# Kernel optimization log

Hardware: AMD Instinct MI355X
Metric: run time of the kernel (lower is better)

The kernel has to match this reference:

```python
import jax, jax.numpy as jnp
import numpy as np

B_GRAPHS, N_PER, T = 64, 5, 256
F_NODE, F_GLOB = 64, 16
H_MSG, H_UPD, H_GRP, H_ACT = 128, 128, 64, 4


def _lstm(x, Wih, Whh, bih, bhh):
    """PyTorch-semantics single-layer LSTM, batch_first=False.
    x: [L, B, Din] -> out [L, B, H]. Scan runs over dim 0 (faithful to the
    original code, which feeds [edges/nodes, T, F] into nn.LSTM)."""
    H = Whh.shape[1]
    xz = jnp.einsum('lbd,gd->lbg', x, Wih) + (bih + bhh)  # precomputed input proj [L,B,4H]
    h0 = jnp.zeros((x.shape[1], H), x.dtype)

    def step(carry, zt):
        h, c = carry
        z = zt + h @ Whh.T
        i, f, g, o = jnp.split(z, 4, axis=-1)  # torch gate order: i,f,g,o
        c = jax.nn.sigmoid(f) * c + jax.nn.sigmoid(i) * jnp.tanh(g)
        h = jax.nn.sigmoid(o) * jnp.tanh(c)
        return (h, c), h

    _, ys = jax.lax.scan(step, (h0, h0), xz)
    return ys


def _forward(nodes, global_attr,
             Wih_m, Whh_m, bih_m, bhh_m,
             Wih_u, Whh_u, bih_u, bhh_u,
             Wih_g, Whh_g, bih_g, bhh_g,
             Wih_a, Whh_a, bih_a, bhh_a,
             edge_indices, num_nodes, num_edges, batch_indices, chosen_who):
    N, Tdim = nodes.shape[0], nodes.shape[1]
    E = edge_indices.shape[1]
    B = num_nodes.shape[0]
    # Faithful to source: both src and target use edge_indices[0]
    src = edge_indices[0]
    tgt = edge_indices[0]
    ga = global_attr.reshape(-1, Tdim, global_attr.shape[1])  # [B, T, G]

    # --- message phase: gather -> LSTM -> relu -> scatter_min ---
    glob_e = jnp.repeat(ga, num_edges, axis=0, total_repeat_length=E)  # [E,T,G]
    msg_in = jnp.concatenate([nodes[src], nodes[tgt], glob_e], axis=2)  # [E,T,2F+G]
    message = jax.nn.relu(_lstm(msg_in, Wih_m, Whh_m, bih_m, bhh_m))    # [E,T,Hm]
    aggr = jax.ops.segment_min(message, tgt, num_segments=N)            # [N,T,Hm]

    # --- node update ---
    glob_n = jnp.repeat(ga, num_nodes, axis=0, total_repeat_length=N)   # [N,T,G]
    upd_in = jnp.concatenate([nodes, aggr, glob_n], axis=2)
    upd = jax.nn.relu(_lstm(upd_in, Wih_u, Whh_u, bih_u, bhh_u))        # [N,T,Hu]

    # --- global / group embedding ---
    agg_nodes = jax.ops.segment_min(upd, batch_indices, num_segments=B) # [B,T,Hu]
    group = jax.nn.relu(_lstm(jnp.concatenate([agg_nodes, ga], axis=2),
                              Wih_g, Whh_g, bih_g, bhh_g))              # [B,T,Hg]

    # --- action head ---
    agg_all = jax.ops.segment_min(upd, batch_indices, num_segments=B)
    counts = jax.ops.segment_sum(jnp.ones_like(batch_indices), batch_indices, num_segments=B)
    offsets = jnp.concatenate([jnp.zeros((1,), counts.dtype), jnp.cumsum(counts)[:-1]])
    adj = jnp.where(chosen_who == 3, chosen_who - 1, chosen_who)
    # faithful: element 0 is NOT adjusted/offset in the original loop
    atbw = jnp.where(jnp.arange(B) == 0, chosen_who, adj + offsets)
    chosen = upd[atbw]                                                  # [B,T,Hu]
    chosen = jnp.where((chosen_who == 3)[:, None, None], agg_all, chosen)
    act_in = jnp.concatenate([chosen, group], axis=2)                   # [B,T,Hu+Hg]
    res = _lstm(act_in, Wih_a, Whh_a, bih_a, bhh_a)[:, -1, :]           # [B, A]
    return jax.nn.softmax(res, axis=1)


def _lstm_params(k, din, h):
    k1, k2, k3, k4 = jax.random.split(k, 4)
    s = 1.0 / np.sqrt(h)
    return (jax.random.uniform(k1, (4 * h, din), jnp.float32, -s, s),
            jax.random.uniform(k2, (4 * h, h), jnp.float32, -s, s),
            jax.random.uniform(k3, (4 * h,), jnp.float32, -s, s),
            jax.random.uniform(k4, (4 * h,), jnp.float32, -s, s))


def setup_inputs() -> dict:
    key = jax.random.key(0)
    ks = jax.random.split(key, 8)
    N = B_GRAPHS * N_PER
    # complete directed graph inside each small group
    src, dst = [], []
    for g in range(B_GRAPHS):
        for i in range(N_PER):
            for j in range(N_PER):
                if i != j:
                    src.append(g * N_PER + i)
                    dst.append(g * N_PER + j)
    edge_indices = jnp.array([src, dst], dtype=jnp.int32)
    inp = {
        'nodes': jax.random.normal(ks[0], (N, T, F_NODE), jnp.float32),
        'global_attr': jax.random.normal(ks[1], (B_GRAPHS * T, F_GLOB), jnp.float32),
        'edge_indices': edge_indices,
        'num_nodes': jnp.full((B_GRAPHS,), N_PER, jnp.int32),
        'num_edges': jnp.full((B_GRAPHS,), N_PER * (N_PER - 1), jnp.int32),
        'batch_indices': jnp.repeat(jnp.arange(B_GRAPHS, dtype=jnp.int32), N_PER),
        'chosen_who': jax.random.randint(ks[2], (B_GRAPHS,), 0, 4, jnp.int32),
    }
    names = [('m', 2 * F_NODE + F_GLOB, H_MSG), ('u', H_MSG + F_NODE + F_GLOB, H_UPD),
             ('g', H_UPD + F_GLOB, H_GRP), ('a', H_UPD + H_GRP, H_ACT)]
    for idx, (suf, din, h) in enumerate(names):
        Wih, Whh, bih, bhh = _lstm_params(ks[3 + idx], din, h)
        inp['Wih_' + suf] = Wih
        inp['Whh_' + suf] = Whh
        inp['bih_' + suf] = bih
        inp['bhh_' + suf] = bhh
    return inp


def reference(nodes, global_attr, edge_indices, num_nodes, num_edges, batch_indices, chosen_who,
              Wih_m, Whh_m, bih_m, bhh_m, Wih_u, Whh_u, bih_u, bhh_u,
              Wih_g, Whh_g, bih_g, bhh_g, Wih_a, Whh_a, bih_a, bhh_a):
    return _forward(nodes, global_attr,
                    Wih_m, Whh_m, bih_m, bhh_m,
                    Wih_u, Whh_u, bih_u, bhh_u,
                    Wih_g, Whh_g, bih_g, bhh_g,
                    Wih_a, Whh_a, bih_a, bhh_a,
                    edge_indices, num_nodes, num_edges, batch_indices, chosen_who)
```

## Files before the change

kernel.cpp:

```cpp
#include <hip/hip_runtime.h>

typedef unsigned int u32;
typedef unsigned short u16;
typedef __fp16 h2 __attribute__((ext_vector_type(2)));

#define BG 64
#define NNODE 320
#define NEDGE 1280
#define TT 256
#define FN 64
#define FG 16
#define HM 128
#define HU 128
#define HG 64
#define HA 4
#define ZM 512
#define ZU 512
#define ZG 256
#define ZA 16
#define DM 144
#define DU 208
#define DG 144
#define DA 192

#define CV 64
#define O_NODES 0
#define O_GA    20480
#define O_WM    21504
#define O_WHM   95232
#define O_BM    160768
#define O_WU    161280
#define O_WHU   267776
#define O_BU    333312
#define O_WG    333824
#define O_WHG   370688
#define O_BG2   387072
#define O_WA    387328
#define O_WHA   390400
#define O_BA    390464
#define CONV_TOTAL 390480
#define O_XZN   390528
#define O_XZU   (O_XZN + NNODE * ZM)
#define O_XZG   (O_XZU + NNODE * ZU)
#define O_XZA   (O_XZG + BG * ZG)
#define O_AGGR  (O_XZA + BG * ZA)
#define O_UPD   (O_AGGR + NNODE * HM)
#define WS_FLOATS (CV + O_UPD + NNODE * HU)

__device__ __forceinline__ float bf2f(u16 v) {
  return __uint_as_float(((u32)v) << 16);
}
__device__ __forceinline__ float rcp_(float x) { return __builtin_amdgcn_rcpf(x); }
__device__ __forceinline__ float sigf(float x) { return rcp_(1.0f + __expf(-x)); }
__device__ __forceinline__ float tanh_(float x) {
  float e = __expf(-2.0f * fabsf(x));
  float t = (1.0f - e) * rcp_(1.0f + e);
  return copysignf(t, x);
}
__device__ __forceinline__ float cvt(const void* p, int i, int flag) {
  return flag ? bf2f(((const u16*)p)[i]) : ((const float*)p)[i];
}

__device__ __forceinline__ h2 pk2(float a, float b) {
  return __builtin_amdgcn_cvt_pkrtz(a, b);
}
__device__ __forceinline__ u32 pk2u(float a, float b) {
  h2 r = __builtin_amdgcn_cvt_pkrtz(a, b);
  u32 out;
  __builtin_memcpy(&out, &r, 4);
  return out;
}

__device__ __forceinline__ float fdot2_(h2 a, h2 b, float c) {
#if __has_builtin(__builtin_amdgcn_fdot2)
  return __builtin_amdgcn_fdot2(a, b, c, false);
#else
  u32 ua, ub;
  __builtin_memcpy(&ua, &a, 4);
  __builtin_memcpy(&ub, &b, 4);
  asm("v_dot2_f32_f16 %0, %1, %2, %0" : "+v"(c) : "v"(ua), "v"(ub));
  return c;
#endif
}

template <int CTRL>
__device__ __forceinline__ float dppmov(float s) {
  return __int_as_float(
      __builtin_amdgcn_update_dpp(0, __float_as_int(s), CTRL, 0xF, 0xF, true));
}

#define BAR() asm volatile("s_waitcnt lgkmcnt(0)\n\ts_barrier" ::: "memory")

__global__ void k_detect(const u32* __restrict__ raw, int* __restrict__ flagp) {
  const int t = threadIdx.x;
  int zlo = 0, hits = 0;
  for (int k = t; k < 256; k += 64) {
    u32 w = raw[k];
    if ((w & 0xFFFFu) == 0u) zlo++;
    u32 m = (w >> 8) & 0x7Fu;
    if (m >= 40u && m <= 70u) hits++;
  }
#pragma unroll
  for (int off = 32; off; off >>= 1) {
    zlo += __shfl_down(zlo, off, 64);
    hits += __shfl_down(hits, off, 64);
  }
  if (t == 0) *flagp = (zlo < 128 && hits >= 128) ? 1 : 0;
}

__global__ __launch_bounds__(256) void k_convert(
    const void* nodes, const void* gattr,
    const void* Wm, const void* Whm, const void* bm1, const void* bm2,
    const void* Wu, const void* Whu, const void* bu1, const void* bu2,
    const void* Wg, const void* Whg, const void* bg1, const void* bg2,
    const void* Wa, const void* Wha, const void* ba1, const void* ba2,
    const int* __restrict__ flagp, float* __restrict__ dst) {
  const int flag = *flagp;
  const int i = blockIdx.x * 256 + threadIdx.x;
  if (i >= CONV_TOTAL) return;
  float v;
  if (i < O_GA) {
    int n = i >> 6, f = i & 63;
    v = cvt(nodes, (n * TT + (TT - 1)) * FN + f, flag);
  } else if (i < O_WM) {
    int l = i - O_GA; int b = l >> 4, g = l & 15;
    v = cvt(gattr, (b * TT + (TT - 1)) * FG + g, flag);
  } else if (i < O_BM) {
    v = (i < O_WHM) ? cvt(Wm, i - O_WM, flag) : cvt(Whm, i - O_WHM, flag);
  } else if (i < O_WU) {
    int l = i - O_BM; v = cvt(bm1, l, flag) + cvt(bm2, l, flag);
  } else if (i < O_BU) {
    v = (i < O_WHU) ? cvt(Wu, i - O_WU, flag) : cvt(Whu, i - O_WHU, flag);
  } else if (i < O_WG) {
    int l = i - O_BU; v = cvt(bu1, l, flag) + cvt(bu2, l, flag);
  } else if (i < O_BG2) {
    v = (i < O_WHG) ? cvt(Wg, i - O_WG, flag) : cvt(Whg, i - O_WHG, flag);
  } else if (i < O_WA) {
    int l = i - O_BG2; v = cvt(bg1, l, flag) + cvt(bg2, l, flag);
  } else if (i < O_WHA) {
    v = cvt(Wa, i - O_WA, flag);
  } else if (i < O_BA) {
    v = cvt(Wha, i - O_WHA, flag);
  } else {
    int l = i - O_BA; v = cvt(ba1, l, flag) + cvt(ba2, l, flag);
  }
  dst[i] = v;
}

__global__ __launch_bounds__(256) void k_pre(
    const float* __restrict__ cva,
    const int* __restrict__ num_nodes,
    float* __restrict__ XZN, float* __restrict__ XZu, float* __restrict__ XZg,
    u32* __restrict__ aggr) {
  const int blk = blockIdx.x, tid = threadIdx.x;
  __shared__ float xv[FN];
  __shared__ float gav[FG];
  __shared__ int sgr;
  const float* nodes255 = cva + O_NODES;
  const float* ga255 = cva + O_GA;

  if (blk < NNODE) {
    const int n = blk;
    if (tid < HM) aggr[(size_t)n * HM + tid] = 0x7f800000u;
    if (tid == 0) {
      int g = 0, acc = 0;
      while (g < BG) { int c = num_nodes[g]; if (n < acc + c) break; acc += c; ++g; }
      if (g >= BG) g = BG - 1;
      sgr = g;
    }
    if (tid < FN) xv[tid] = nodes255[n * FN + tid];
    __syncthreads();
    if (tid < FG) gav[tid] = ga255[sgr * FG + tid];
    __syncthreads();
    for (int j = tid; j < ZM; j += 256) {
      const float* wr = cva + O_WM + j * DM;
      float acc = cva[O_BM + j];
#pragma unroll
      for (int d = 0; d < FN; ++d) acc += (wr[d] + wr[FN + d]) * xv[d];
#pragma unroll
      for (int d = 0; d < FG; ++d) acc += wr[2 * FN + d] * gav[d];
      XZN[(size_t)n * ZM + j] = acc;
    }
  } else if (blk < 2 * NNODE) {
    const int n = blk - NNODE;
    if (tid == 0) {
      int g = 0, acc = 0;
      while (g < BG) { int c = num_nodes[g]; if (n < acc + c) break; acc += c; ++g; }
      if (g >= BG) g = BG - 1;
      sgr = g;
    }
    if (tid < FN) xv[tid] = nodes255[n * FN + tid];
    __syncthreads();
    if (tid < FG) gav[tid] = ga255[sgr * FG + tid];
    __syncthreads();
    for (int j = tid; j < ZU; j += 256) {
      const float* wr = cva + O_WU + j * DU;
      float acc = cva[O_BU + j];
#pragma unroll
      for (int d = 0; d < FN; ++d) acc += wr[d] * xv[d];
#pragma unroll
      for (int d = 0; d < FG; ++d) acc += wr[FN + HM + d] * gav[d];
      XZu[(size_t)n * ZU + j] = acc;
    }
  } else {
    const int b = blk - 2 * NNODE;
    if (tid < FG) gav[tid] = ga255[b * FG + tid];
    __syncthreads();
    if (tid < ZG) {
      const float* wr = cva + O_WG + tid * DG;
      float acc = cva[O_BG2 + tid];
#pragma unroll
      for (int d = 0; d < FG; ++d) acc += wr[HU + d] * gav[d];
      XZg[(size_t)b * ZG + tid] = acc;
    }
  }
}

template <int STEPS, bool GATHER, bool ATOMIN>
__global__ __launch_bounds__(512, 2) void k_chain(
    const float* __restrict__ Whh, const float* __restrict__ XZ,
    const int* __restrict__ idx, float* __restrict__ hout) {
  const int t = threadIdx.x;
  const int p = t & 3;
  const int elem = t >> 2;
  const bool islead = (p == 0);
  __shared__ u32 hbuf[2][80];

  h2 w16[64];
  {
    const float4* wr = (const float4*)(Whh + (size_t)(p * 128 + elem) * 128);
#pragma unroll
    for (int q = 0; q < 32; ++q) {
      float4 v = wr[q];
      w16[2 * q] = pk2(v.x, v.y);
      w16[2 * q + 1] = pk2(v.z, v.w);
    }
  }
  const float LOG2E = 1.4426950408889634f;
  const float kmul = (p == 2) ? (-2.0f * LOG2E) : (-LOG2E);
  const float smul = (p == 2) ? 2.0f : 1.0f;
  const float badd = (p == 2) ? -1.0f : 0.0f;
  const float KT2 = -2.0f * LOG2E;

  if (t < 160) ((u32*)hbuf)[t] = 0u;
  float c = 0.0f;
  float hrelu_prev = 0.0f;
  int crow = GATHER ? idx[0] : 0;
  float xz = XZ[(size_t)crow * 512 + p * 128 + elem];
  int nrow = GATHER ? idx[1] : 1;
  BAR();
  int cur = 0;
  for (int e = 0; e < STEPS; ++e) {
    const uint4* hb = (const uint4*)&hbuf[cur][0];
    float a0 = 0.0f, a1 = 0.0f, a2 = 0.0f, a3 = 0.0f;
#pragma unroll
    for (int q = 0; q < 16; ++q) {
      uint4 tv = hb[q];
      h2 h0, h1, h2_, h3;
      __builtin_memcpy(&h0, &tv.x, 4);
      __builtin_memcpy(&h1, &tv.y, 4);
      __builtin_memcpy(&h2_, &tv.z, 4);
      __builtin_memcpy(&h3, &tv.w, 4);
      a0 = fdot2_(w16[4 * q + 0], h0, a0);
      a1 = fdot2_(w16[4 * q + 1], h1, a1);
      a2 = fdot2_(w16[4 * q + 2], h2_, a2);
      a3 = fdot2_(w16[4 * q + 3], h3, a3);
    }
    float z = ((a0 + a1) + (a2 + a3)) + xz;
    float xzn = XZ[(size_t)nrow * 512 + p * 128 + elem];
    int crow_next = nrow;
    nrow = GATHER ? idx[e + 2] : (e + 2);
    float ex = __builtin_amdgcn_exp2f(z * kmul);
    float gq = __builtin_fmaf(smul, rcp_(1.0f + ex), badd);
    float gf = dppmov<0xB1>(gq);
    float gt = dppmov<0x4E>(gq);
    float go = dppmov<0x1B>(gq);
    c = __builtin_fmaf(gf, c, gq * gt);
    float ec = __builtin_amdgcn_exp2f(c * KT2);
    float th = __builtin_fmaf(2.0f, rcp_(1.0f + ec), -1.0f);
    float h = go * th;
    if (islead) {
      ((u16*)&hbuf[cur ^ 1][0])[elem] = (u16)pk2u(h, h);
      float hr = fmaxf(h, 0.0f);
      if (ATOMIN) {
        atomicMin((u32*)&hout[(size_t)crow * HM + elem], __float_as_uint(hr));
      } else {
        if (e > 0) hout[(size_t)(e - 1) * 128 + elem] = hrelu_prev;
        hrelu_prev = hr;
      }
    }
    crow = crow_next;
    xz = xzn;
    BAR();
    cur ^= 1;
  }
  if (islead && !ATOMIN) hout[(size_t)(STEPS - 1) * 128 + elem] = hrelu_prev;
}

__global__ __launch_bounds__(256) void k_aggproj(
    const float* __restrict__ cva, const float* __restrict__ aggr,
    float* __restrict__ XZu) {
  const int n = blockIdx.x, tid = threadIdx.x;
  __shared__ float av[HM];
  if (tid < HM) av[tid] = aggr[(size_t)n * HM + tid];
  __syncthreads();
  for (int j = tid; j < ZU; j += 256) {
    const float* wr = cva + O_WU + j * DU + FN;
    float acc = 0.0f;
#pragma unroll
    for (int k = 0; k < HM; ++k) acc += wr[k] * av[k];
    XZu[(size_t)n * ZU + j] += acc;
  }
}

__global__ __launch_bounds__(256) void k_gproj(
    const float* __restrict__ cva, const float* __restrict__ upd,
    const int* __restrict__ bidx, const int* __restrict__ who,
    float* __restrict__ XZg, float* __restrict__ XZa) {
  const int blk = blockIdx.x, tid = threadIdx.x;
  __shared__ float buf[HU];
  __shared__ int satbw;
  if (blk < BG) {
    const int b = blk;
    if (tid < HU) {
      float m = __uint_as_float(0x7f800000u);
      for (int n = 0; n < NNODE; ++n) {
        if (bidx[n] == b) m = fminf(m, upd[(size_t)n * HU + tid]);
      }
      buf[tid] = m;
    }
    __syncthreads();
    if (tid < ZG) {
      const float* wr = cva + O_WG + tid * DG;
      float acc = 0.0f;
#pragma unroll
      for (int k = 0; k < HU; ++k) acc += wr[k] * buf[k];
      XZg[(size_t)b * ZG + tid] += acc;
    }
  } else {
    const int b = blk - BG;
    const int whoB = who[b];
    if (tid == 0) {
      int off = 0;
      for (int i = 0; i < NNODE; ++i) off += (bidx[i] < b) ? 1 : 0;
      const int adj = (whoB == 3) ? 2 : whoB;
      satbw = (b == 0) ? who[0] : (adj + off);
    }
    if (whoB == 3) {
      if (tid < HU) {
        float m = __uint_as_float(0x7f800000u);
        for (int n = 0; n < NNODE; ++n) {
          if (bidx[n] == b) m = fminf(m, upd[(size_t)n * HU + tid]);
        }
        buf[tid] = m;
      }
      __syncthreads();
    } else {
      __syncthreads();
      if (tid < HU) buf[tid] = upd[(size_t)satbw * HU + tid];
      __syncthreads();
    }
    if (tid < ZA) {
      const float* wr = cva + O_WA + tid * DA;
      float acc = cva[O_BA + tid];
#pragma unroll
      for (int k = 0; k < HU; ++k) acc += wr[k] * buf[k];
      XZa[(size_t)b * ZA + tid] = acc;
    }
  }
}

__global__ __launch_bounds__(256, 2) void k_final(
    const float* __restrict__ cva, const float* __restrict__ XZg,
    const float* __restrict__ XZa, float* __restrict__ out) {
  const int j = threadIdx.x;
  __shared__ __align__(16) float hg[HG];
  __shared__ float zsg[ZG];
  __shared__ float grp[BG * HG];
  __shared__ float za[ZA];
  __shared__ float haL[HA];
  __shared__ float res[BG * HA];

  float wg[HG];
  {
    const float* wr = cva + O_WHG + j * HG;
#pragma unroll
    for (int k = 0; k < HG; ++k) wg[k] = wr[k];
  }
  float wa2[HG];
  float wha[HA];
  if (j < ZA) {
    const float* wr2 = cva + O_WA + j * DA + HU;
#pragma unroll
    for (int k = 0; k < HG; ++k) wa2[k] = wr2[k];
#pragma unroll
    for (int k = 0; k < HA; ++k) wha[k] = cva[O_WHA + j * HA + k];
  }
  if (j < HG) hg[j] = 0.0f;
  if (j < HA) haL[j] = 0.0f;
  float cg = 0.0f, ca = 0.0f;
  __syncthreads();

  for (int b = 0; b <= BG; ++b) {
    if (b < BG) {
      float acc = XZg[(size_t)b * ZG + j];
#pragma unroll
      for (int k = 0; k < HG; ++k) acc += wg[k] * hg[k];
      zsg[j] = acc;
    }
    if (b > 0 && j < ZA) {
      float acc = XZa[(size_t)(b - 1) * ZA + j];
#pragma unroll
      for (int k = 0; k < HG; ++k) acc += wa2[k] * grp[(b - 1) * HG + k];
#pragma unroll
      for (int k = 0; k < HA; ++k) acc += wha[k] * haL[k];
      za[j] = acc;
    }
    __syncthreads();
    if (b < BG && j < HG) {
      float zi = zsg[j], zf = zsg[HG + j], zg = zsg[2 * HG + j], zo = zsg[3 * HG + j];
      cg = sigf(zf) * cg + sigf(zi) * tanh_(zg);
      float h = sigf(zo) * tanh_(cg);
      hg[j] = h;
      grp[b * HG + j] = fmaxf(h, 0.0f);
    }
    if (b > 0 && j < HA) {
      float zi = za[j], zf = za[HA + j], zg = za[2 * HA + j], zo = za[3 * HA + j];
      ca = sigf(zf) * ca + sigf(zi) * tanh_(zg);
      float h = sigf(zo) * tanh_(ca);
      haL[j] = h;
      res[(b - 1) * HA + j] = h;
    }
    __syncthreads();
  }

  if (j < BG) {
    float x0 = res[j * 4 + 0], x1 = res[j * 4 + 1];
    float x2 = res[j * 4 + 2], x3 = res[j * 4 + 3];
    float m = fmaxf(fmaxf(x0, x1), fmaxf(x2, x3));
    float e0 = __expf(x0 - m), e1 = __expf(x1 - m);
    float e2 = __expf(x2 - m), e3 = __expf(x3 - m);
    float s = e0 + e1 + e2 + e3;
    out[j * 4 + 0] = e0 / s;
    out[j * 4 + 1] = e1 / s;
    out[j * 4 + 2] = e2 / s;
    out[j * 4 + 3] = e3 / s;
  }
}

__global__ void k_zero(float* out) { out[threadIdx.x] = 0.0f; }

extern "C" void kernel_launch(void* const* d_in, const int* in_sizes, int n_in,
                              void* d_out, int out_size, void* d_ws, size_t ws_size,
                              hipStream_t stream) {
  const void* nodes = d_in[0];
  const void* gattr = d_in[1];
  const int* eidx  = (const int*)d_in[2];
  const int* nn    = (const int*)d_in[3];
  const int* ne    = (const int*)d_in[4];
  const int* bidx  = (const int*)d_in[5];
  const int* who   = (const int*)d_in[6];
  (void)ne;

  if (ws_size < (size_t)WS_FLOATS * 4) {
    k_zero<<<1, 256, 0, stream>>>((float*)d_out);
    return;
  }

  float* ws = (float*)d_ws;
  int* flagp = (int*)d_ws;
  float* cva = ws + CV;
  float* XZN = cva + O_XZN;
  float* XZu = cva + O_XZU;
  float* XZg = cva + O_XZG;
  float* XZa = cva + O_XZA;
  float* aggr = cva + O_AGGR;
  float* upd = cva + O_UPD;

  k_detect<<<1, 64, 0, stream>>>((const u32*)nodes, flagp);
  k_convert<<<(CONV_TOTAL + 255) / 256, 256, 0, stream>>>(
      nodes, gattr,
      d_in[7], d_in[8], d_in[9], d_in[10],
      d_in[11], d_in[12], d_in[13], d_in[14],
      d_in[15], d_in[16], d_in[17], d_in[18],
      d_in[19], d_in[20], d_in[21], d_in[22],
      flagp, cva);
  k_pre<<<2 * NNODE + BG, 256, 0, stream>>>(cva, nn, XZN, XZu, XZg, (u32*)aggr);
  k_chain<NEDGE, true, true><<<1, 512, 0, stream>>>(cva + O_WHM, XZN, eidx, aggr);
  k_aggproj<<<NNODE, 256, 0, stream>>>(cva, aggr, XZu);
  k_chain<NNODE, false, false><<<1, 512, 0, stream>>>(cva + O_WHU, XZu, nullptr, upd);
  k_gproj<<<2 * BG, 256, 0, stream>>>(cva, upd, bidx, who, XZg, XZa);
  k_final<<<1, 256, 0, stream>>>(cva, XZg, XZa, (float*)d_out);
}
```

Before: 1.124 ms.

## Compute LSTM recurrent matvec with MFMA and interleave gate layout

Replaces the per-thread fdot2 recurrent matvec in the sequential LSTM chain kernel with MFMA 16x16x32 f16 instructions. The weights are held as A fragments and the hidden vector is broadcast as the B operand. Gate pre-activations go through shared memory to 128 cell threads, and the XZ projections are stored gate-interleaved so each cell thread loads its four gates as one float4. This adds a second barrier per step and wastes most MFMA columns (only one useful column). Latency per step may improve or worsen.

```diff
diff --git a/kernel.cpp b/kernel.cpp
--- a/kernel.cpp
+++ b/kernel.cpp
@@ -2,7 +2,8 @@
 
 typedef unsigned int u32;
 typedef unsigned short u16;
-typedef __fp16 h2 __attribute__((ext_vector_type(2)));
+typedef __fp16 h8 __attribute__((ext_vector_type(8)));
+typedef float f32x4 __attribute__((ext_vector_type(4)));
 
 #define BG 64
 #define NNODE 320
@@ -60,33 +61,11 @@
 __device__ __forceinline__ float cvt(const void* p, int i, int flag) {
   return flag ? bf2f(((const u16*)p)[i]) : ((const float*)p)[i];
 }
-
-__device__ __forceinline__ h2 pk2(float a, float b) {
-  return __builtin_amdgcn_cvt_pkrtz(a, b);
-}
-__device__ __forceinline__ u32 pk2u(float a, float b) {
-  h2 r = __builtin_amdgcn_cvt_pkrtz(a, b);
+__device__ __forceinline__ u16 f2h(float a) {
+  auto r = __builtin_amdgcn_cvt_pkrtz(a, a);
   u32 out;
   __builtin_memcpy(&out, &r, 4);
-  return out;
-}
-
-__device__ __forceinline__ float fdot2_(h2 a, h2 b, float c) {
-#if __has_builtin(__builtin_amdgcn_fdot2)
-  return __builtin_amdgcn_fdot2(a, b, c, false);
-#else
-  u32 ua, ub;
-  __builtin_memcpy(&ua, &a, 4);
-  __builtin_memcpy(&ub, &b, 4);
-  asm("v_dot2_f32_f16 %0, %1, %2, %0" : "+v"(c) : "v"(ua), "v"(ub));
-  return c;
-#endif
-}
-
-template <int CTRL>
-__device__ __forceinline__ float dppmov(float s) {
-  return __int_as_float(
-      __builtin_amdgcn_update_dpp(0, __float_as_int(s), CTRL, 0xF, 0xF, true));
+  return (u16)out;
 }
 
 #define BAR() asm volatile("s_waitcnt lgkmcnt(0)\n\ts_barrier" ::: "memory")
@@ -179,7 +158,7 @@
       for (int d = 0; d < FN; ++d) acc += (wr[d] + wr[FN + d]) * xv[d];
 #pragma unroll
       for (int d = 0; d < FG; ++d) acc += wr[2 * FN + d] * gav[d];
-      XZN[(size_t)n * ZM + j] = acc;
+      XZN[(size_t)n * ZM + (j & 127) * 4 + (j >> 7)] = acc;
     }
   } else if (blk < 2 * NNODE) {
     const int n = blk - NNODE;
@@ -200,7 +179,7 @@
       for (int d = 0; d < FN; ++d) acc += wr[d] * xv[d];
 #pragma unroll
       for (int d = 0; d < FG; ++d) acc += wr[FN + HM + d] * gav[d];
-      XZu[(size_t)n * ZU + j] = acc;
+      XZu[(size_t)n * ZU + (j & 127) * 4 + (j >> 7)] = acc;
     }
   } else {
     const int b = blk - 2 * NNODE;
@@ -221,80 +200,95 @@
     const float* __restrict__ Whh, const float* __restrict__ XZ,
     const int* __restrict__ idx, float* __restrict__ hout) {
   const int t = threadIdx.x;
-  const int p = t & 3;
-  const int elem = t >> 2;
-  const bool islead = (p == 0);
-  __shared__ u32 hbuf[2][80];
-
-  h2 w16[64];
+  const int lane = t & 63;
+  const int wv = t >> 6;
+  const bool iscell = (t < 128);
+  __shared__ __align__(16) u16 hlds[136];
+  __shared__ __align__(16) float zlds[512];
+
+  h8 wfrag[16];
   {
-    const float4* wr = (const float4*)(Whh + (size_t)(p * 128 + elem) * 128);
-#pragma unroll
-    for (int q = 0; q < 32; ++q) {
-      float4 v = wr[q];
-      w16[2 * q] = pk2(v.x, v.y);
-      w16[2 * q + 1] = pk2(v.z, v.w);
-    }
-  }
-  const float LOG2E = 1.4426950408889634f;
-  const float kmul = (p == 2) ? (-2.0f * LOG2E) : (-LOG2E);
-  const float smul = (p == 2) ? 2.0f : 1.0f;
-  const float badd = (p == 2) ? -1.0f : 0.0f;
-  const float KT2 = -2.0f * LOG2E;
-
-  if (t < 160) ((u32*)hbuf)[t] = 0u;
-  float c = 0.0f;
-  float hrelu_prev = 0.0f;
-  int crow = GATHER ? idx[0] : 0;
-  float xz = XZ[(size_t)crow * 512 + p * 128 + elem];
-  int nrow = GATHER ? idx[1] : 1;
+    const int vr = lane & 15;
+    const int kb = (lane >> 4) * 8;
+#pragma unroll
+    for (int mm = 0; mm < 4; ++mm) {
+      const int m = wv * 4 + mm;
+      const int vrow = 16 * m + vr;
+      const int elem = vrow >> 2;
+      const int p = vrow & 3;
+      const float* row = Whh + (size_t)(p * 128 + elem) * 128;
+#pragma unroll
+      for (int c = 0; c < 4; ++c) {
+        float4 lo = *(const float4*)(row + 32 * c + kb);
+        float4 hi = *(const float4*)(row + 32 * c + kb + 4);
+        h8 f;
+        f[0] = (__fp16)lo.x; f[1] = (__fp16)lo.y;
+        f[2] = (__fp16)lo.z; f[3] = (__fp16)lo.w;
+        f[4] = (__fp16)hi.x; f[5] = (__fp16)hi.y;
+        f[6] = (__fp16)hi.z; f[7] = (__fp16)hi.w;
+        wfrag[mm * 4 + c] = f;
+      }
+    }
+  }
+
+  float cst = 0.0f;
+  int crow = 0, nrow = 1;
+  f32x4 xz = {0.0f, 0.0f, 0.0f, 0.0f};
+  if (iscell) {
+    crow = GATHER ? idx[0] : 0;
+    nrow = GATHER ? idx[1] : 1;
+    xz = *(const f32x4*)(XZ + (size_t)crow * 512 + t * 4);
+  }
+  if (t < 136) hlds[t] = 0;
   BAR();
-  int cur = 0;
+
   for (int e = 0; e < STEPS; ++e) {
-    const uint4* hb = (const uint4*)&hbuf[cur][0];
-    float a0 = 0.0f, a1 = 0.0f, a2 = 0.0f, a3 = 0.0f;
-#pragma unroll
-    for (int q = 0; q < 16; ++q) {
-      uint4 tv = hb[q];
-      h2 h0, h1, h2_, h3;
-      __builtin_memcpy(&h0, &tv.x, 4);
-      __builtin_memcpy(&h1, &tv.y, 4);
-      __builtin_memcpy(&h2_, &tv.z, 4);
-      __builtin_memcpy(&h3, &tv.w, 4);
-      a0 = fdot2_(w16[4 * q + 0], h0, a0);
-      a1 = fdot2_(w16[4 * q + 1], h1, a1);
-      a2 = fdot2_(w16[4 * q + 2], h2_, a2);
-      a3 = fdot2_(w16[4 * q + 3], h3, a3);
-    }
-    float z = ((a0 + a1) + (a2 + a3)) + xz;
-    float xzn = XZ[(size_t)nrow * 512 + p * 128 + elem];
-    int crow_next = nrow;
-    nrow = GATHER ? idx[e + 2] : (e + 2);
-    float ex = __builtin_amdgcn_exp2f(z * kmul);
-    float gq = __builtin_fmaf(smul, rcp_(1.0f + ex), badd);
-    float gf = dppmov<0xB1>(gq);
-    float gt = dppmov<0x4E>(gq);
-    float go = dppmov<0x1B>(gq);
-    c = __builtin_fmaf(gf, c, gq * gt);
-    float ec = __builtin_amdgcn_exp2f(c * KT2);
-    float th = __builtin_fmaf(2.0f, rcp_(1.0f + ec), -1.0f);
-    float h = go * th;
-    if (islead) {
-      ((u16*)&hbuf[cur ^ 1][0])[elem] = (u16)pk2u(h, h);
+    h8 bf[4];
+#pragma unroll
+    for (int c = 0; c < 4; ++c) {
+      uint4 v = *(const uint4*)((const char*)hlds + 64 * c + ((lane >> 4) & 3) * 16);
+      __builtin_memcpy(&bf[c], &v, 16);
+    }
+    f32x4 d0 = {0.0f, 0.0f, 0.0f, 0.0f};
+    f32x4 d1 = d0, d2 = d0, d3 = d0;
+#pragma unroll
+    for (int c = 0; c < 4; ++c) {
+      d0 = __builtin_amdgcn_mfma_f32_16x16x32_f16(wfrag[0 * 4 + c], bf[c], d0, 0, 0, 0);
+      d1 = __builtin_amdgcn_mfma_f32_16x16x32_f16(wfrag[1 * 4 + c], bf[c], d1, 0, 0, 0);
+      d2 = __builtin_amdgcn_mfma_f32_16x16x32_f16(wfrag[2 * 4 + c], bf[c], d2, 0, 0, 0);
+      d3 = __builtin_amdgcn_mfma_f32_16x16x32_f16(wfrag[3 * 4 + c], bf[c], d3, 0, 0, 0);
+    }
+    if ((lane & 15) == 0) {
+      const int rb = (lane >> 4) * 4;
+      *(f32x4*)&zlds[16 * (wv * 4 + 0) + rb] = d0;
+      *(f32x4*)&zlds[16 * (wv * 4 + 1) + rb] = d1;
+      *(f32x4*)&zlds[16 * (wv * 4 + 2) + rb] = d2;
+      *(f32x4*)&zlds[16 * (wv * 4 + 3) + rb] = d3;
+    }
+    BAR();
+    if (iscell) {
+      f32x4 z = *(const f32x4*)&zlds[t * 4];
+      float zi = z[0] + xz[0], zf = z[1] + xz[1];
+      float zg = z[2] + xz[2], zo = z[3] + xz[3];
+      int crow_next = nrow;
+      f32x4 xzn = *(const f32x4*)(XZ + (size_t)nrow * 512 + t * 4);
+      nrow = GATHER ? idx[e + 2] : (e + 2);
+      float si = sigf(zi), sf = sigf(zf), so = sigf(zo);
+      float tg = tanh_(zg);
+      cst = sf * cst + si * tg;
+      float h = so * tanh_(cst);
+      hlds[t] = f2h(h);
       float hr = fmaxf(h, 0.0f);
       if (ATOMIN) {
-        atomicMin((u32*)&hout[(size_t)crow * HM + elem], __float_as_uint(hr));
+        atomicMin((u32*)&hout[(size_t)crow * HM + t], __float_as_uint(hr));
       } else {
-        if (e > 0) hout[(size_t)(e - 1) * 128 + elem] = hrelu_prev;
-        hrelu_prev = hr;
+        hout[(size_t)e * 128 + t] = hr;
       }
-    }
-    crow = crow_next;
-    xz = xzn;
+      crow = crow_next;
+      xz = xzn;
+    }
     BAR();
-    cur ^= 1;
-  }
-  if (islead && !ATOMIN) hout[(size_t)(STEPS - 1) * 128 + elem] = hrelu_prev;
+  }
 }
 
 __global__ __launch_bounds__(256) void k_aggproj(
@@ -309,7 +303,7 @@
     float acc = 0.0f;
 #pragma unroll
     for (int k = 0; k < HM; ++k) acc += wr[k] * av[k];
-    XZu[(size_t)n * ZU + j] += acc;
+    XZu[(size_t)n * ZU + (j & 127) * 4 + (j >> 7)] += acc;
   }
 }
 
```

Result: slower. 1.394 ms (+23.9%).
